# Optimization experiments

Hardware: AMD Instinct MI355X
Metric: run time of the kernel (lower is better)

Reference implementation:

```python
import jax, jax.numpy as jnp
import numpy as np

B, QL, DL = 256, 16, 512      # batch, query len, doc graph nodes
ND, NW, ED = 512, 50000, 300  # n_docs, vocab, embed dim
TOPK, K2, K4 = 40, 240, 192   # args.topk, ggnn2 keep, ggnn4 keep


def setup_inputs() -> dict:
    key = jax.random.key(0)
    ks = jax.random.split(key, 32)
    s = 0.1
    inp = {
        "emb": jax.random.normal(ks[0], (NW + 1, ED), jnp.float32),
        "qrl_token": jax.random.randint(ks[1], (B, QL), 0, NW),
        "doc_token": jax.random.randint(ks[2], (B, DL), 0, NW),
        "doc_ids": jax.random.randint(ks[3], (B,), 0, ND),
        "docs_adj": jax.random.uniform(ks[4], (ND, DL, DL), jnp.float32),
        "idf": jax.random.uniform(ks[5], (B, QL, 1), jnp.float32),
        "W_g1": jax.random.normal(ks[6], (6, QL, QL), jnp.float32) * s,
        "b_g1": jax.random.normal(ks[7], (6, QL), jnp.float32) * s,
        "w_g2": jax.random.normal(ks[8], (6,), jnp.float32) * s,
        "b_g2": jax.random.normal(ks[9], (6,), jnp.float32) * s,
        "W_g3": jax.random.normal(ks[10], (6, QL, QL), jnp.float32) * s,
        "b_g3": jax.random.normal(ks[11], (6, QL), jnp.float32) * s,
        "w_g4": jax.random.normal(ks[12], (6,), jnp.float32) * s,
        "b_g4": jax.random.normal(ks[13], (6,), jnp.float32) * s,
        "p1_w": jax.random.normal(ks[14], (QL,), jnp.float32) * s,
        "p1_b": jax.random.normal(ks[15], (1,), jnp.float32) * s,
        "p2_w": jax.random.normal(ks[16], (QL,), jnp.float32) * s,
        "p2_b": jax.random.normal(ks[17], (1,), jnp.float32) * s,
        "l1_w": jax.random.normal(ks[18], (64, 3 * TOPK), jnp.float32) * s,
        "l1_b": jax.random.normal(ks[19], (64,), jnp.float32) * s,
        "l2_w": jax.random.normal(ks[20], (32, 64), jnp.float32) * s,
        "l2_b": jax.random.normal(ks[21], (32,), jnp.float32) * s,
        "l3_w": jax.random.normal(ks[22], (1, 32), jnp.float32) * s,
        "l3_b": jax.random.normal(ks[23], (1,), jnp.float32) * s,
        "gated_w": jax.random.normal(ks[24], (1,), jnp.float32) * s,
        "gated_b": jax.random.normal(ks[25], (1,), jnp.float32) * s,
    }
    return inp


def _simmat(a_emb, b_emb):
    # cosine similarity [B, A, C]
    an = jnp.linalg.norm(a_emb, axis=2)[:, :, None] + 1e-9
    bn = jnp.linalg.norm(b_emb, axis=2)[:, None, :] + 1e-9
    return jnp.einsum("bad,bcd->bac", a_emb, b_emb) / (an * bn)


def _gate_mat(a, x, W, b):
    # GGNN gated update, W: [6, D, D] stacked (z0,z1,r0,r1,h0,h1)
    lin = lambda t, i: t @ W[i].T + b[i]
    z = jax.nn.sigmoid(lin(a, 0) + lin(x, 1))
    r = jax.nn.sigmoid(lin(a, 2) + lin(x, 3))
    h = jax.nn.relu(lin(a, 4) + lin(r * x, 5))
    return h * z + x * (1.0 - z)


def _gate_scalar(a, x, w, b):
    lin = lambda t, i: t * w[i] + b[i]
    z = jax.nn.sigmoid(lin(a, 0) + lin(x, 1))
    r = jax.nn.sigmoid(lin(a, 2) + lin(x, 3))
    h = jax.nn.relu(lin(a, 4) + lin(r * x, 5))
    return h * z + x * (1.0 - z)


def _sub_adj(A, idx):
    # A: [L, L], idx: [K] -> A[idx][:, idx]
    return A[idx][:, idx]


def reference(emb, qrl_token, doc_token, doc_ids, docs_adj, idf,
              W_g1, b_g1, w_g2, b_g2, W_g3, b_g3, w_g4, b_g4,
              p1_w, p1_b, p2_w, p2_b,
              l1_w, l1_b, l2_w, l2_b, l3_w, l3_b, gated_w, gated_b):
    qe = emb[qrl_token]               # [B, QL, ED]
    de = emb[doc_token]               # [B, DL, ED]
    feat = _simmat(qe, de).transpose(0, 2, 1)   # [B, DL, QL]
    topk0 = jax.lax.top_k(feat.transpose(0, 2, 1), TOPK)[0]  # [B, QL, TOPK]

    adj = docs_adj[doc_ids]           # [B, DL, DL]

    # ggnn1
    rep1 = _gate_mat(adj @ feat, feat, W_g1, b_g1)           # [B, DL, QL]

    # ggnn2 (scalar gates on projected feature + topk subgraph gather)
    x2 = rep1 @ p1_w[:, None] + p1_b                         # [B, DL, 1]
    feat_s = _gate_scalar(adj @ x2, x2, w_g2, b_g2)          # [B, DL, 1]
    score1, idx1 = jax.lax.top_k(feat_s[..., 0], K2)         # [B, K2]
    att_x1 = jnp.take_along_axis(rep1, idx1[:, :, None], axis=1)  # [B, K2, QL]
    adj_new = jax.vmap(_sub_adj)(adj, idx1)                  # [B, K2, K2]
    att_x1 = jnp.tanh(score1)[:, :, None] * att_x1

    # ggnn3
    rep3 = _gate_mat(adj_new @ att_x1, att_x1, W_g3, b_g3)   # [B, K2, QL]

    # ggnn4
    x4 = rep3 @ p2_w[:, None] + p2_b                         # [B, K2, 1]
    feat_s4 = _gate_scalar(adj_new @ x4, x4, w_g4, b_g4)
    score2, idx2 = jax.lax.top_k(feat_s4[..., 0], K4)        # [B, K4]
    att_x2 = jnp.take_along_axis(rep3, idx2[:, :, None], axis=1)  # [B, K4, QL]
    att_x2 = jnp.tanh(score2)[:, :, None] * att_x2

    att1 = jax.lax.top_k(att_x1.transpose(0, 2, 1), TOPK)[0]  # [B, QL, TOPK]
    att2 = jax.lax.top_k(att_x2.transpose(0, 2, 1), TOPK)[0]  # [B, QL, TOPK]
    att_x = jnp.concatenate([topk0, att1, att2], axis=-1)     # [B, QL, 3*TOPK]

    rel = jax.nn.relu(att_x @ l1_w.T + l1_b)
    rel = jax.nn.relu(rel @ l2_w.T + l2_b)
    rel = rel @ l3_w.T + l3_b                                 # [B, QL, 1]

    gated_weight = jax.nn.softmax(idf * gated_w + gated_b, axis=1)
    rel = rel * gated_weight
    scores = rel[..., 0].sum(-1, keepdims=True)               # [B, 1]
    return scores
```

## Files before the change

### kernel.cpp

```cpp
#include <hip/hip_runtime.h>
#include <math.h>

#define B_   256
#define QL_  16
#define DL_  512
#define ED_  300
#define K2_  240
#define K4_  192
#define NEGINF (-3.402823466e38f)

__device__ __forceinline__ float sigf(float x){ return 1.0f/(1.0f+__expf(-x)); }

__device__ __forceinline__ float dot16(const float (&a)[16], const float* w){
  float s = 0.f;
  #pragma unroll
  for (int i=0;i<4;i++){
    float4 ww = *(const float4*)(w + 4*i);
    s = fmaf(a[4*i+0], ww.x, s);
    s = fmaf(a[4*i+1], ww.y, s);
    s = fmaf(a[4*i+2], ww.z, s);
    s = fmaf(a[4*i+3], ww.w, s);
  }
  return s;
}

template<int N, int T>
__device__ void bitonic_desc(float* v, int* id){
  const int tid = threadIdx.x;
  for (int k = 2; k <= N; k <<= 1){
    for (int j = k >> 1; j > 0; j >>= 1){
      __syncthreads();
      for (int i = tid; i < N; i += T){
        const int l = i ^ j;
        if (l > i){
          const float vi = v[i], vl = v[l];
          const int ii = id[i], il = id[l];
          const bool before_l = (vl > vi) || (vl == vi && il < ii);
          const bool up = ((i & k) == 0);
          if (up == before_l){ v[i]=vl; v[l]=vi; id[i]=il; id[l]=ii; }
        }
      }
    }
  }
  __syncthreads();
}

template<int NREG>
__device__ __forceinline__ void wave_sort_desc(float (&v)[NREG], int lane){
  constexpr int TOT = NREG*64;
  #pragma unroll
  for (int k = 2; k <= TOT; k <<= 1){
    #pragma unroll
    for (int j = k>>1; j > 0; j >>= 1){
      if (j >= 64){
        const int jr = j >> 6;
        #pragma unroll
        for (int r = 0; r < NREG; r++){
          if ((r & jr) == 0){
            const int p = r | jr;
            const bool desc = (((r*64) & k) == 0);
            const float a = v[r], c = v[p];
            const float mx = fmaxf(a,c), mn = fminf(a,c);
            v[r] = desc ? mx : mn;
            v[p] = desc ? mn : mx;
          }
        }
      } else {
        #pragma unroll
        for (int r = 0; r < NREG; r++){
          const float ov = __shfl_xor(v[r], j);
          const bool desc = (((r*64 + lane) & k) == 0);
          const bool lower = (lane & j) == 0;
          v[r] = (lower == desc) ? fmaxf(v[r], ov) : fminf(v[r], ov);
        }
      }
    }
  }
}

__global__ __launch_bounds__(1024) void k_all(
    const float* __restrict__ emb, const int* __restrict__ qtok,
    const int* __restrict__ dtok, const int* __restrict__ dids,
    const float* __restrict__ dadj,
    const float* __restrict__ Wg1, const float* __restrict__ bg1,
    const float* __restrict__ p1w, const float* __restrict__ p1b,
    const float* __restrict__ wg2, const float* __restrict__ bg2,
    const float* __restrict__ Wg3, const float* __restrict__ bg3,
    const float* __restrict__ p2w, const float* __restrict__ p2b,
    const float* __restrict__ wg4, const float* __restrict__ bg4,
    const float* __restrict__ l1w, const float* __restrict__ l1b,
    const float* __restrict__ l2w, const float* __restrict__ l2b,
    const float* __restrict__ l3w, const float* __restrict__ l3b,
    const float* __restrict__ idf, const float* __restrict__ gw,
    const float* __restrict__ gb,
    float* __restrict__ adjnew, float* __restrict__ outp)
{
  extern __shared__ float sm[];
  float* ql   = sm;
  float* fx   = ql + 4864;
  float* repl = fx + 10240;
  float* wl   = repl + 10240;
  float* bl   = wl + 1536;
  float* pwl  = bl + 96;
  float* xv   = pwl + 16;
  float* sval = xv + 512;
  int*   sidx = (int*)(sval + 512);
  int*   il   = sidx + 512;
  float* attl = (float*)(il + 240);
  float* rel1 = attl + 1920;
  float* rel2 = rel1 + 1024;
  float* qinv = rel2 + 512;
  int*   toks = (int*)(qinv + 16);

  const int tid = threadIdx.x, b = blockIdx.x;
  const int wave = tid >> 6, lane = tid & 63;
  const float* abase = dadj + (size_t)dids[b]*512*512;

  for (int idx = tid; idx < 16*ED_; idx += 1024){
    const int q = idx / ED_, e = idx - q*ED_;
    ql[q*304+e] = emb[(size_t)qtok[(size_t)b*QL_ + q]*ED_ + e];
  }
  if (tid < 512) toks[tid] = dtok[(size_t)b*DL_ + tid];
  for (int idx = tid; idx < 1536; idx += 1024) wl[idx] = Wg1[idx];
  if (tid >= 1024-96 && tid < 1024) bl[tid-(1024-96)] = bg1[tid-(1024-96)];
  if (tid >= 512 && tid < 528) pwl[tid-512] = p1w[tid-512];
  __syncthreads();
  if (tid < 256){
    const int q = tid >> 4, s = tid & 15;
    float ss = 0.f;
    for (int e=s;e<ED_;e+=16){ const float x = ql[q*304+e]; ss = fmaf(x,x,ss); }
    ss += __shfl_xor(ss,1); ss += __shfl_xor(ss,2);
    ss += __shfl_xor(ss,4); ss += __shfl_xor(ss,8);
    if (s == 0) qinv[q] = 1.f/(sqrtf(ss)+1e-9f);
  }
  __syncthreads();

  {
    const int g = tid>>2, sub = tid&3;
    const float* e0p = emb + (size_t)toks[2*g+0]*ED_;
    const float* e1p = emb + (size_t)toks[2*g+1]*ED_;
    float acc[2][16];
    float ssr[2] = {0.f,0.f};
    #pragma unroll
    for (int r=0;r<2;r++)
      #pragma unroll
      for (int q=0;q<16;q++) acc[r][q] = 0.f;
    for (int i=0;i<19;i++){
      const int j = sub + 4*i;
      if (j < 75){
        const int e0 = 4*j;
        float4 d0v = *(const float4*)(e0p + e0);
        float4 d1v = *(const float4*)(e1p + e0);
        ssr[0] = fmaf(d0v.x,d0v.x, fmaf(d0v.y,d0v.y, fmaf(d0v.z,d0v.z, fmaf(d0v.w,d0v.w, ssr[0]))));
        ssr[1] = fmaf(d1v.x,d1v.x, fmaf(d1v.y,d1v.y, fmaf(d1v.z,d1v.z, fmaf(d1v.w,d1v.w, ssr[1]))));
        #pragma unroll
        for (int q=0;q<16;q++){
          float4 qv = *(const float4*)(&ql[q*304 + e0]);
          acc[0][q] = fmaf(d0v.x,qv.x, fmaf(d0v.y,qv.y, fmaf(d0v.z,qv.z, fmaf(d0v.w,qv.w, acc[0][q]))));
          acc[1][q] = fmaf(d1v.x,qv.x, fmaf(d1v.y,qv.y, fmaf(d1v.z,qv.z, fmaf(d1v.w,qv.w, acc[1][q]))));
        }
      }
    }
    #pragma unroll
    for (int r=0;r<2;r++){
      #pragma unroll
      for (int q=0;q<16;q++){
        float v = acc[r][q];
        v += __shfl_xor(v, 1);
        v += __shfl_xor(v, 2);
        acc[r][q] = v;
      }
      float sv = ssr[r];
      sv += __shfl_xor(sv, 1);
      sv += __shfl_xor(sv, 2);
      ssr[r] = sv;
    }
    if (sub < 2){
      const int d = 2*g + sub;
      const float ssd = sub ? ssr[1] : ssr[0];
      const float invd = 1.f/(sqrtf(ssd)+1e-9f);
      float vs[16];
      #pragma unroll
      for (int q=0;q<16;q++){
        const float v = sub ? acc[1][q] : acc[0][q];
        vs[q] = v * invd * qinv[q];
      }
      float* fo = &fx[(size_t)d*20];
      *(float4*)(fo+0)  = make_float4(vs[0],vs[1],vs[2],vs[3]);
      *(float4*)(fo+4)  = make_float4(vs[4],vs[5],vs[6],vs[7]);
      *(float4*)(fo+8)  = make_float4(vs[8],vs[9],vs[10],vs[11]);
      *(float4*)(fo+12) = make_float4(vs[12],vs[13],vs[14],vs[15]);
    }
  }
  __syncthreads();

  {
    const int q = wave;
    float v[8];
    #pragma unroll
    for (int r=0;r<8;r++) v[r] = fx[(size_t)(lane + 64*r)*20 + q];
    wave_sort_desc<8>(v, lane);
    if (lane < 40) attl[q*120 + lane] = v[0];
  }

  {
    const int g = tid>>2, sub = tid&3;
    const int mb = 2*g;
    const float* r0 = abase + (size_t)mb * 512;
    float acc[2][16];
    #pragma unroll
    for (int r=0;r<2;r++)
      #pragma unroll
      for (int q=0;q<16;q++) acc[r][q] = 0.f;
    for (int i = 0; i < 32; i++){
      const int kk = i*16 + sub*4;
      float4 a0 = *(const float4*)(r0 + kk);
      float4 a1 = *(const float4*)(r0 + 512 + kk);
      const float av[2][4] = {{a0.x,a0.y,a0.z,a0.w},{a1.x,a1.y,a1.z,a1.w}};
      #pragma unroll
      for (int c = 0; c < 4; c++){
        const float* fr = &fx[(size_t)(kk + c)*20];
        float4 q0 = *(const float4*)(fr);
        float4 q1 = *(const float4*)(fr+4);
        float4 q2 = *(const float4*)(fr+8);
        float4 q3 = *(const float4*)(fr+12);
        const float qv[16] = {q0.x,q0.y,q0.z,q0.w, q1.x,q1.y,q1.z,q1.w,
                              q2.x,q2.y,q2.z,q2.w, q3.x,q3.y,q3.z,q3.w};
        #pragma unroll
        for (int r = 0; r < 2; r++){
          const float a_ = av[r][c];
          #pragma unroll
          for (int q = 0; q < 16; q++)
            acc[r][q] = fmaf(a_, qv[q], acc[r][q]);
        }
      }
    }
    #pragma unroll
    for (int r=0;r<2;r++)
      #pragma unroll
      for (int q=0;q<16;q++){
        float v = acc[r][q];
        v += __shfl_xor(v, 1);
        v += __shfl_xor(v, 2);
        acc[r][q] = v;
      }
    if (sub < 2){
      const int m = mb + sub;
      float a[16], x[16];
      #pragma unroll
      for (int q=0;q<16;q++)
        a[q] = sub ? acc[1][q] : acc[0][q];
      {
        const float* xr = &fx[(size_t)m*20];
        float4 x0 = *(const float4*)(xr),   x1 = *(const float4*)(xr+4);
        float4 x2v = *(const float4*)(xr+8), x3 = *(const float4*)(xr+12);
        x[0]=x0.x; x[1]=x0.y; x[2]=x0.z; x[3]=x0.w;
        x[4]=x1.x; x[5]=x1.y; x[6]=x1.z; x[7]=x1.w;
        x[8]=x2v.x; x[9]=x2v.y; x[10]=x2v.z; x[11]=x2v.w;
        x[12]=x3.x; x[13]=x3.y; x[14]=x3.z; x[15]=x3.w;
      }
      float z[16], rr[16];
      #pragma unroll
      for (int q=0;q<16;q++){
        const float s0 = bl[q] + bl[16+q]
                       + dot16(a, &wl[q*16]) + dot16(x, &wl[256 + q*16]);
        z[q] = sigf(s0);
        const float s1 = bl[32+q] + bl[48+q]
                       + dot16(a, &wl[512 + q*16]) + dot16(x, &wl[768 + q*16]);
        rr[q] = sigf(s1);
      }
      float rx[16];
      #pragma unroll
      for (int q=0;q<16;q++) rx[q] = rr[q]*x[q];
      float out[16]; float xp = 0.f;
      #pragma unroll
      for (int q=0;q<16;q++){
        const float s = bl[64+q] + bl[80+q]
                      + dot16(a, &wl[1024 + q*16]) + dot16(rx, &wl[1280 + q*16]);
        const float h = fmaxf(s, 0.f);
        const float o = h*z[q] + x[q]*(1.f - z[q]);
        out[q] = o;
        xp = fmaf(o, pwl[q], xp);
      }
      float* rp = &repl[(size_t)m*20];
      *(float4*)(rp+0)  = make_float4(out[0],out[1],out[2],out[3]);
      *(float4*)(rp+4)  = make_float4(out[4],out[5],out[6],out[7]);
      *(float4*)(rp+8)  = make_float4(out[8],out[9],out[10],out[11]);
      *(float4*)(rp+12) = make_float4(out[12],out[13],out[14],out[15]);
      xv[m] = xp + p1b[0];
    }
  }
  __syncthreads();

  {
    const int g = tid >> 2, sub = tid & 3;
    const float w0=wg2[0],w1=wg2[1],w2=wg2[2],w3=wg2[3],w4=wg2[4],w5=wg2[5];
    const float c0=bg2[0],c1=bg2[1],c2=bg2[2],c3=bg2[3],c4=bg2[4],c5=bg2[5];
    #pragma unroll
    for (int pp=0; pp<2; pp++){
      const int m = pp*256 + g;
      const float* row = abase + (size_t)m*512;
      float s = 0.f;
      #pragma unroll
      for (int ii=0; ii<8; ii++){
        const int k0 = ii*64 + sub*4;
        float4 a0 = *(const float4*)(row + k0);
        float4 a1 = *(const float4*)(row + k0 + 16);
        float4 a2 = *(const float4*)(row + k0 + 32);
        float4 a3 = *(const float4*)(row + k0 + 48);
        float4 x0 = *(const float4*)(&xv[k0]);
        float4 x1 = *(const float4*)(&xv[k0+16]);
        float4 x2v = *(const float4*)(&xv[k0+32]);
        float4 x3 = *(const float4*)(&xv[k0+48]);
        s = fmaf(a0.x,x0.x,s); s = fmaf(a0.y,x0.y,s);
        s = fmaf(a0.z,x0.z,s); s = fmaf(a0.w,x0.w,s);
        s = fmaf(a1.x,x1.x,s); s = fmaf(a1.y,x1.y,s);
        s = fmaf(a1.z,x1.z,s); s = fmaf(a1.w,x1.w,s);
        s = fmaf(a2.x,x2v.x,s); s = fmaf(a2.y,x2v.y,s);
        s = fmaf(a2.z,x2v.z,s); s = fmaf(a2.w,x2v.w,s);
        s = fmaf(a3.x,x3.x,s); s = fmaf(a3.y,x3.y,s);
        s = fmaf(a3.z,x3.z,s); s = fmaf(a3.w,x3.w,s);
      }
      s += __shfl_xor(s,1); s += __shfl_xor(s,2);
      if (sub == 0){
        const float x = xv[m];
        const float z = sigf(fmaf(s,w0,c0) + fmaf(x,w1,c1));
        const float r = sigf(fmaf(s,w2,c2) + fmaf(x,w3,c3));
        const float h = fmaxf(fmaf(s,w4,c4) + fmaf(r*x,w5,c5), 0.f);
        sval[m] = h*z + x*(1.f - z);
        sidx[m] = m;
      }
    }
  }
  bitonic_desc<512,1024>(sval, sidx);

  if (tid < K2_){
    const int rowi = sidx[tid];
    il[tid] = rowi;
    const float tv = tanhf(sval[tid]);
    const float* rr = &repl[(size_t)rowi*20];
    float4 r0 = *(const float4*)(rr),   r1 = *(const float4*)(rr+4);
    float4 r2 = *(const float4*)(rr+8), r3 = *(const float4*)(rr+12);
    float* o = &fx[(size_t)tid*20];
    *(float4*)(o+0)  = make_float4(tv*r0.x,tv*r0.y,tv*r0.z,tv*r0.w);
    *(float4*)(o+4)  = make_float4(tv*r1.x,tv*r1.y,tv*r1.z,tv*r1.w);
    *(float4*)(o+8)  = make_float4(tv*r2.x,tv*r2.y,tv*r2.z,tv*r2.w);
    *(float4*)(o+12) = make_float4(tv*r3.x,tv*r3.y,tv*r3.z,tv*r3.w);
  }
  __syncthreads();

  if (wave < 12){
    int jc[4];
    #pragma unroll
    for (int c=0;c<4;c++){
      const int j = lane + 64*c;
      jc[c] = (j < K2_) ? il[j] : 0;
    }
    #pragma unroll
    for (int p=0;p<20;p++){
      const int r = wave*20 + p;
      const float* row = abase + (size_t)il[r]*512;
      float* orow = adjnew + ((size_t)b*K2_ + r)*K2_;
      #pragma unroll
      for (int c=0;c<4;c++){
        const int j = lane + 64*c;
        if (j < K2_) orow[j] = row[jc[c]];
      }
    }
  } else {
    const int t4 = tid - 768;
    for (int idx = t4; idx < 1536; idx += 256) wl[idx] = Wg3[idx];
    if (t4 < 96) bl[t4] = bg3[t4];
    if (t4 < 16) pwl[t4] = p2w[t4];
    #pragma unroll
    for (int t=0;t<4;t++){
      const int q = (wave-12)*4 + t;
      float v[4];
      #pragma unroll
      for (int r=0;r<4;r++){
        const int idx = lane + 64*r;
        v[r] = (idx < K2_) ? fx[(size_t)idx*20 + q] : NEGINF;
      }
      wave_sort_desc<4>(v, lane);
      if (lane < 40) attl[q*120 + 40 + lane] = v[0];
    }
  }
  __syncthreads();

  {
    const int g = tid >> 2, sub = tid & 3;
    if (g < K2_){
      const int m = g;
      const float* r0 = adjnew + ((size_t)b*K2_ + m)*K2_;
      float acc[16];
      #pragma unroll
      for (int q=0;q<16;q++) acc[q] = 0.f;
      for (int i=0;i<15;i++){
        const int kk = i*16 + sub*4;
        float4 a4 = *(const float4*)(r0 + kk);
        const float av[4] = {a4.x, a4.y, a4.z, a4.w};
        #pragma unroll
        for (int c=0;c<4;c++){
          const float* fr = &fx[(size_t)(kk + c)*20];
          float4 q0 = *(const float4*)(fr);
          float4 q1 = *(const float4*)(fr+4);
          float4 q2 = *(const float4*)(fr+8);
          float4 q3 = *(const float4*)(fr+12);
          const float qv[16] = {q0.x,q0.y,q0.z,q0.w, q1.x,q1.y,q1.z,q1.w,
                                q2.x,q2.y,q2.z,q2.w, q3.x,q3.y,q3.z,q3.w};
          #pragma unroll
          for (int q=0;q<16;q++)
            acc[q] = fmaf(av[c], qv[q], acc[q]);
        }
      }
      #pragma unroll
      for (int q=0;q<16;q++){
        float v = acc[q];
        v += __shfl_xor(v, 1);
        v += __shfl_xor(v, 2);
        acc[q] = v;
      }
      float x[16];
      {
        const float* xr = &fx[(size_t)m*20];
        float4 x0 = *(const float4*)(xr),   x1 = *(const float4*)(xr+4);
        float4 x2v = *(const float4*)(xr+8), x3 = *(const float4*)(xr+12);
        x[0]=x0.x; x[1]=x0.y; x[2]=x0.z; x[3]=x0.w;
        x[4]=x1.x; x[5]=x1.y; x[6]=x1.z; x[7]=x1.w;
        x[8]=x2v.x; x[9]=x2v.y; x[10]=x2v.z; x[11]=x2v.w;
        x[12]=x3.x; x[13]=x3.y; x[14]=x3.z; x[15]=x3.w;
      }
      float rx[16];
      #pragma unroll
      for (int q=0;q<16;q++){
        const float s1 = bl[32+q] + bl[48+q]
                       + dot16(acc, &wl[512 + q*16]) + dot16(x, &wl[768 + q*16]);
        rx[q] = sigf(s1) * x[q];
      }
      float xp = 0.f;
      #pragma unroll
      for (int j=0;j<4;j++){
        const int q = sub*4 + j;
        const float s0 = bl[q] + bl[16+q]
                       + dot16(acc, &wl[q*16]) + dot16(x, &wl[256 + q*16]);
        const float z = sigf(s0);
        const float s = bl[64+q] + bl[80+q]
                      + dot16(acc, &wl[1024 + q*16]) + dot16(rx, &wl[1280 + q*16]);
        const float h = fmaxf(s, 0.f);
        const float o = h*z + x[q]*(1.f - z);
        repl[(size_t)m*20 + q] = o;
        xp = fmaf(o, pwl[q], xp);
      }
      xp += __shfl_xor(xp,1); xp += __shfl_xor(xp,2);
      if (sub == 0) xv[m] = xp + p2b[0];
    }
  }
  __syncthreads();

  {
    const int g = tid >> 2, sub = tid & 3;
    const float w0=wg4[0],w1=wg4[1],w2=wg4[2],w3=wg4[3],w4=wg4[4],w5=wg4[5];
    const float c0=bg4[0],c1=bg4[1],c2=bg4[2],c3=bg4[3],c4=bg4[4],c5=bg4[5];
    if (g < K2_){
      const float* row = adjnew + ((size_t)b*K2_ + g)*K2_;
      float s = 0.f;
      #pragma unroll
      for (int i=0;i<15;i++){
        const int kk = i*16 + sub*4;
        float4 a4 = *(const float4*)(row + kk);
        float4 xq = *(const float4*)(&xv[kk]);
        s = fmaf(a4.x,xq.x,s); s = fmaf(a4.y,xq.y,s);
        s = fmaf(a4.z,xq.z,s); s = fmaf(a4.w,xq.w,s);
      }
      s += __shfl_xor(s,1); s += __shfl_xor(s,2);
      if (sub == 0){
        const float x = xv[g];
        const float z = sigf(fmaf(s,w0,c0) + fmaf(x,w1,c1));
        const float r = sigf(fmaf(s,w2,c2) + fmaf(x,w3,c3));
        const float h = fmaxf(fmaf(s,w4,c4) + fmaf(r*x,w5,c5), 0.f);
        sval[g] = h*z + x*(1.f - z);
        sidx[g] = g;
      }
    }
    if (tid >= 960 && tid < 976){
      sval[K2_ + tid - 960] = NEGINF;
      sidx[K2_ + tid - 960] = 0x7fffffff;
    }
  }
  bitonic_desc<256,1024>(sval, sidx);

  if (tid < K4_){
    const int rowi = sidx[tid];
    const float tv = tanhf(sval[tid]);
    const float* rr = &repl[(size_t)rowi*20];
    float4 r0 = *(const float4*)(rr),   r1 = *(const float4*)(rr+4);
    float4 r2 = *(const float4*)(rr+8), r3 = *(const float4*)(rr+12);
    float* o = &fx[(size_t)tid*20];
    *(float4*)(o+0)  = make_float4(tv*r0.x,tv*r0.y,tv*r0.z,tv*r0.w);
    *(float4*)(o+4)  = make_float4(tv*r1.x,tv*r1.y,tv*r1.z,tv*r1.w);
    *(float4*)(o+8)  = make_float4(tv*r2.x,tv*r2.y,tv*r2.z,tv*r2.w);
    *(float4*)(o+12) = make_float4(tv*r3.x,tv*r3.y,tv*r3.z,tv*r3.w);
  }
  __syncthreads();

  {
    const int q = wave;
    float v[4];
    #pragma unroll
    for (int r=0;r<4;r++){
      const int idx = lane + 64*r;
      v[r] = (idx < K4_) ? fx[(size_t)idx*20 + q] : NEGINF;
    }
    wave_sort_desc<4>(v, lane);
    if (lane < 40) attl[q*120 + 80 + lane] = v[0];
  }
  __syncthreads();

  {
    const int q = tid >> 6, u = tid & 63;
    float acc = l1b[u];
    const float* wrow = l1w + (size_t)u*120;
    #pragma unroll
    for (int k4=0;k4<30;k4++){
      float4 av = *(const float4*)(&attl[q*120 + k4*4]);
      float4 wv = *(const float4*)(wrow + k4*4);
      acc = fmaf(av.x,wv.x,acc); acc = fmaf(av.y,wv.y,acc);
      acc = fmaf(av.z,wv.z,acc); acc = fmaf(av.w,wv.w,acc);
    }
    rel1[q*64 + u] = fmaxf(acc, 0.f);
  }
  __syncthreads();
  if (tid < 512){
    const int q = tid >> 5, u = tid & 31;
    float acc = l2b[u];
    const float* wrow = l2w + (size_t)u*64;
    #pragma unroll
    for (int k4=0;k4<16;k4++){
      float4 av = *(const float4*)(&rel1[q*64 + k4*4]);
      float4 wv = *(const float4*)(wrow + k4*4);
      acc = fmaf(av.x,wv.x,acc); acc = fmaf(av.y,wv.y,acc);
      acc = fmaf(av.z,wv.z,acc); acc = fmaf(av.w,wv.w,acc);
    }
    rel2[q*32 + u] = fmaxf(acc, 0.f);
  }
  __syncthreads();
  if (tid < 16){
    float acc = l3b[0];
    #pragma unroll
    for (int k=0;k<32;k++) acc = fmaf(rel2[tid*32+k], l3w[k], acc);
    const float gv = fmaf(idf[(size_t)b*16 + tid], gw[0], gb[0]);
    float mx = gv;
    mx = fmaxf(mx, __shfl_xor(mx, 1));
    mx = fmaxf(mx, __shfl_xor(mx, 2));
    mx = fmaxf(mx, __shfl_xor(mx, 4));
    mx = fmaxf(mx, __shfl_xor(mx, 8));
    const float e = __expf(gv - mx);
    float se = e;
    se += __shfl_xor(se, 1); se += __shfl_xor(se, 2);
    se += __shfl_xor(se, 4); se += __shfl_xor(se, 8);
    float val = acc * (e / se);
    val += __shfl_xor(val, 1); val += __shfl_xor(val, 2);
    val += __shfl_xor(val, 4); val += __shfl_xor(val, 8);
    if (tid == 0) outp[b] = val;
  }
}

extern "C" void kernel_launch(void* const* d_in, const int* in_sizes, int n_in,
                              void* d_out, int out_size, void* d_ws, size_t ws_size,
                              hipStream_t stream)
{
  const float* emb  = (const float*)d_in[0];
  const int*   qtok = (const int*)d_in[1];
  const int*   dtok = (const int*)d_in[2];
  const int*   dids = (const int*)d_in[3];
  const float* dadj = (const float*)d_in[4];
  const float* idf  = (const float*)d_in[5];
  const float* Wg1  = (const float*)d_in[6];
  const float* bg1  = (const float*)d_in[7];
  const float* wg2  = (const float*)d_in[8];
  const float* bg2  = (const float*)d_in[9];
  const float* Wg3  = (const float*)d_in[10];
  const float* bg3  = (const float*)d_in[11];
  const float* wg4  = (const float*)d_in[12];
  const float* bg4  = (const float*)d_in[13];
  const float* p1w  = (const float*)d_in[14];
  const float* p1b  = (const float*)d_in[15];
  const float* p2w  = (const float*)d_in[16];
  const float* p2b  = (const float*)d_in[17];
  const float* l1w  = (const float*)d_in[18];
  const float* l1b  = (const float*)d_in[19];
  const float* l2w  = (const float*)d_in[20];
  const float* l2b  = (const float*)d_in[21];
  const float* l3w  = (const float*)d_in[22];
  const float* l3b  = (const float*)d_in[23];
  const float* gw   = (const float*)d_in[24];
  const float* gb   = (const float*)d_in[25];
  float* out = (float*)d_out;

  float* adjnew = (float*)d_ws;

  const size_t lds_bytes = 32740u * 4u;

  k_all<<<B_, 1024, lds_bytes, stream>>>(
      emb, qtok, dtok, dids, dadj,
      Wg1, bg1, p1w, p1b, wg2, bg2, Wg3, bg3, p2w, p2b, wg4, bg4,
      l1w, l1b, l2w, l2b, l3w, l3b, idf, gw, gb,
      adjnew, out);
}
```

Baseline: 235.3 us.

## Prefetch embedding and adjacency rows, specialize waves for GGNN1 versus top-k sort

Embedding row loads in the similarity stage are software-pipelined two iterations ahead. The GGNN1 adjacency matmul is now done by the first 8 waves, each thread group handling 4 rows with a one-step register prefetch. The remaining waves run the per-query top-k sorts (two queries each) at the same time, so the work is split across waves instead of running in sequence. This raises register pressure (4x16 accumulators) and cuts the number of waves doing the matmul, which risks lower occupancy and longer GGNN1 time. The prefetch in the embedding loop also reads past the valid range on the last iterations, which may touch memory beyond the row.

Result: slower. 283.3 us (+20.4%).

```diff
diff --git a/kernel.cpp b/kernel.cpp
--- a/kernel.cpp
+++ b/kernel.cpp
@@ -145,21 +145,27 @@
     for (int r=0;r<2;r++)
       #pragma unroll
       for (int q=0;q<16;q++) acc[r][q] = 0.f;
+    float4 a0 = *(const float4*)(e0p + 4*(sub));
+    float4 a1 = *(const float4*)(e1p + 4*(sub));
+    float4 b0 = *(const float4*)(e0p + 4*(sub+4));
+    float4 b1 = *(const float4*)(e1p + 4*(sub+4));
     for (int i=0;i<19;i++){
+      const int jn = sub + 4*(i+2);
+      float4 c0v = *(const float4*)(e0p + 4*jn);
+      float4 c1v = *(const float4*)(e1p + 4*jn);
       const int j = sub + 4*i;
       if (j < 75){
         const int e0 = 4*j;
-        float4 d0v = *(const float4*)(e0p + e0);
-        float4 d1v = *(const float4*)(e1p + e0);
-        ssr[0] = fmaf(d0v.x,d0v.x, fmaf(d0v.y,d0v.y, fmaf(d0v.z,d0v.z, fmaf(d0v.w,d0v.w, ssr[0]))));
-        ssr[1] = fmaf(d1v.x,d1v.x, fmaf(d1v.y,d1v.y, fmaf(d1v.z,d1v.z, fmaf(d1v.w,d1v.w, ssr[1]))));
+        ssr[0] = fmaf(a0.x,a0.x, fmaf(a0.y,a0.y, fmaf(a0.z,a0.z, fmaf(a0.w,a0.w, ssr[0]))));
+        ssr[1] = fmaf(a1.x,a1.x, fmaf(a1.y,a1.y, fmaf(a1.z,a1.z, fmaf(a1.w,a1.w, ssr[1]))));
         #pragma unroll
         for (int q=0;q<16;q++){
           float4 qv = *(const float4*)(&ql[q*304 + e0]);
-          acc[0][q] = fmaf(d0v.x,qv.x, fmaf(d0v.y,qv.y, fmaf(d0v.z,qv.z, fmaf(d0v.w,qv.w, acc[0][q]))));
-          acc[1][q] = fmaf(d1v.x,qv.x, fmaf(d1v.y,qv.y, fmaf(d1v.z,qv.z, fmaf(d1v.w,qv.w, acc[1][q]))));
+          acc[0][q] = fmaf(a0.x,qv.x, fmaf(a0.y,qv.y, fmaf(a0.z,qv.z, fmaf(a0.w,qv.w, acc[0][q]))));
+          acc[1][q] = fmaf(a1.x,qv.x, fmaf(a1.y,qv.y, fmaf(a1.z,qv.z, fmaf(a1.w,qv.w, acc[1][q]))));
         }
       }
+      a0 = b0; a1 = b1; b0 = c0v; b1 = c1v;
     }
     #pragma unroll
     for (int r=0;r<2;r++){
@@ -194,29 +200,28 @@
   }
   __syncthreads();
 
-  {
-    const int q = wave;
-    float v[8];
-    #pragma unroll
-    for (int r=0;r<8;r++) v[r] = fx[(size_t)(lane + 64*r)*20 + q];
-    wave_sort_desc<8>(v, lane);
-    if (lane < 40) attl[q*120 + lane] = v[0];
-  }
-
-  {
-    const int g = tid>>2, sub = tid&3;
-    const int mb = 2*g;
+  if (wave < 8){
+    const int g = tid >> 2, sub = tid & 3;
+    const int mb = 4*g;
     const float* r0 = abase + (size_t)mb * 512;
-    float acc[2][16];
-    #pragma unroll
-    for (int r=0;r<2;r++)
+    float acc[4][16];
+    #pragma unroll
+    for (int r=0;r<4;r++)
       #pragma unroll
       for (int q=0;q<16;q++) acc[r][q] = 0.f;
+    int kk = sub*4;
+    float4 c0 = *(const float4*)(r0 + kk);
+    float4 c1 = *(const float4*)(r0 + 512 + kk);
+    float4 c2 = *(const float4*)(r0 + 2*512 + kk);
+    float4 c3 = *(const float4*)(r0 + 3*512 + kk);
     for (int i = 0; i < 32; i++){
-      const int kk = i*16 + sub*4;
-      float4 a0 = *(const float4*)(r0 + kk);
-      float4 a1 = *(const float4*)(r0 + 512 + kk);
-      const float av[2][4] = {{a0.x,a0.y,a0.z,a0.w},{a1.x,a1.y,a1.z,a1.w}};
+      const int kn = kk + ((i < 31) ? 16 : 0);
+      float4 n0 = *(const float4*)(r0 + kn);
+      float4 n1 = *(const float4*)(r0 + 512 + kn);
+      float4 n2 = *(const float4*)(r0 + 2*512 + kn);
+      float4 n3 = *(const float4*)(r0 + 3*512 + kn);
+      const float av[4][4] = {{c0.x,c0.y,c0.z,c0.w},{c1.x,c1.y,c1.z,c1.w},
+                              {c2.x,c2.y,c2.z,c2.w},{c3.x,c3.y,c3.z,c3.w}};
       #pragma unroll
       for (int c = 0; c < 4; c++){
         const float* fr = &fx[(size_t)(kk + c)*20];
@@ -227,16 +232,18 @@
         const float qv[16] = {q0.x,q0.y,q0.z,q0.w, q1.x,q1.y,q1.z,q1.w,
                               q2.x,q2.y,q2.z,q2.w, q3.x,q3.y,q3.z,q3.w};
         #pragma unroll
-        for (int r = 0; r < 2; r++){
+        for (int r = 0; r < 4; r++){
           const float a_ = av[r][c];
           #pragma unroll
           for (int q = 0; q < 16; q++)
             acc[r][q] = fmaf(a_, qv[q], acc[r][q]);
         }
       }
-    }
-    #pragma unroll
-    for (int r=0;r<2;r++)
+      c0 = n0; c1 = n1; c2 = n2; c3 = n3;
+      kk += 16;
+    }
+    #pragma unroll
+    for (int r=0;r<4;r++)
       #pragma unroll
       for (int q=0;q<16;q++){
         float v = acc[r][q];
@@ -244,50 +251,58 @@
         v += __shfl_xor(v, 2);
         acc[r][q] = v;
       }
-    if (sub < 2){
-      const int m = mb + sub;
-      float a[16], x[16];
-      #pragma unroll
-      for (int q=0;q<16;q++)
-        a[q] = sub ? acc[1][q] : acc[0][q];
-      {
-        const float* xr = &fx[(size_t)m*20];
-        float4 x0 = *(const float4*)(xr),   x1 = *(const float4*)(xr+4);
-        float4 x2v = *(const float4*)(xr+8), x3 = *(const float4*)(xr+12);
-        x[0]=x0.x; x[1]=x0.y; x[2]=x0.z; x[3]=x0.w;
-        x[4]=x1.x; x[5]=x1.y; x[6]=x1.z; x[7]=x1.w;
-        x[8]=x2v.x; x[9]=x2v.y; x[10]=x2v.z; x[11]=x2v.w;
-        x[12]=x3.x; x[13]=x3.y; x[14]=x3.z; x[15]=x3.w;
-      }
-      float z[16], rr[16];
-      #pragma unroll
-      for (int q=0;q<16;q++){
-        const float s0 = bl[q] + bl[16+q]
-                       + dot16(a, &wl[q*16]) + dot16(x, &wl[256 + q*16]);
-        z[q] = sigf(s0);
-        const float s1 = bl[32+q] + bl[48+q]
-                       + dot16(a, &wl[512 + q*16]) + dot16(x, &wl[768 + q*16]);
-        rr[q] = sigf(s1);
-      }
-      float rx[16];
-      #pragma unroll
-      for (int q=0;q<16;q++) rx[q] = rr[q]*x[q];
-      float out[16]; float xp = 0.f;
-      #pragma unroll
-      for (int q=0;q<16;q++){
-        const float s = bl[64+q] + bl[80+q]
-                      + dot16(a, &wl[1024 + q*16]) + dot16(rx, &wl[1280 + q*16]);
-        const float h = fmaxf(s, 0.f);
-        const float o = h*z[q] + x[q]*(1.f - z[q]);
-        out[q] = o;
-        xp = fmaf(o, pwl[q], xp);
-      }
-      float* rp = &repl[(size_t)m*20];
-      *(float4*)(rp+0)  = make_float4(out[0],out[1],out[2],out[3]);
-      *(float4*)(rp+4)  = make_float4(out[4],out[5],out[6],out[7]);
-      *(float4*)(rp+8)  = make_float4(out[8],out[9],out[10],out[11]);
-      *(float4*)(rp+12) = make_float4(out[12],out[13],out[14],out[15]);
-      xv[m] = xp + p1b[0];
+    const int m = mb + sub;
+    float a[16], x[16];
+    #pragma unroll
+    for (int q=0;q<16;q++)
+      a[q] = (sub==0)?acc[0][q]:(sub==1)?acc[1][q]:(sub==2)?acc[2][q]:acc[3][q];
+    {
+      const float* xr = &fx[(size_t)m*20];
+      float4 x0 = *(const float4*)(xr),   x1 = *(const float4*)(xr+4);
+      float4 x2v = *(const float4*)(xr+8), x3 = *(const float4*)(xr+12);
+      x[0]=x0.x; x[1]=x0.y; x[2]=x0.z; x[3]=x0.w;
+      x[4]=x1.x; x[5]=x1.y; x[6]=x1.z; x[7]=x1.w;
+      x[8]=x2v.x; x[9]=x2v.y; x[10]=x2v.z; x[11]=x2v.w;
+      x[12]=x3.x; x[13]=x3.y; x[14]=x3.z; x[15]=x3.w;
+    }
+    float z[16], rr[16];
+    #pragma unroll
+    for (int q=0;q<16;q++){
+      const float s0 = bl[q] + bl[16+q]
+                     + dot16(a, &wl[q*16]) + dot16(x, &wl[256 + q*16]);
+      z[q] = sigf(s0);
+      const float s1 = bl[32+q] + bl[48+q]
+                     + dot16(a, &wl[512 + q*16]) + dot16(x, &wl[768 + q*16]);
+      rr[q] = sigf(s1);
+    }
+    float rx[16];
+    #pragma unroll
+    for (int q=0;q<16;q++) rx[q] = rr[q]*x[q];
+    float out[16]; float xp = 0.f;
+    #pragma unroll
+    for (int q=0;q<16;q++){
+      const float s = bl[64+q] + bl[80+q]
+                    + dot16(a, &wl[1024 + q*16]) + dot16(rx, &wl[1280 + q*16]);
+      const float h = fmaxf(s, 0.f);
+      const float o = h*z[q] + x[q]*(1.f - z[q]);
+      out[q] = o;
+      xp = fmaf(o, pwl[q], xp);
+    }
+    float* rp = &repl[(size_t)m*20];
+    *(float4*)(rp+0)  = make_float4(out[0],out[1],out[2],out[3]);
+    *(float4*)(rp+4)  = make_float4(out[4],out[5],out[6],out[7]);
+    *(float4*)(rp+8)  = make_float4(out[8],out[9],out[10],out[11]);
+    *(float4*)(rp+12) = make_float4(out[12],out[13],out[14],out[15]);
+    xv[m] = xp + p1b[0];
+  } else {
+    #pragma unroll
+    for (int t=0;t<2;t++){
+      const int q = (wave-8)*2 + t;
+      float v[8];
+      #pragma unroll
+      for (int r=0;r<8;r++) v[r] = fx[(size_t)(lane + 64*r)*20 + q];
+      wave_sort_desc<8>(v, lane);
+      if (lane < 40) attl[q*120 + lane] = v[0];
     }
   }
   __syncthreads();
```

## Use register/shuffle hybrid bitonic sort and transposed LDS buffers for top-k

Applied to the files above, without the earlier changes.

The shared-memory bitonic sort, which synchronised on every stage, is replaced by a register-held sort. Partner exchanges with stride below 64 use wave shuffles and only larger strides go through LDS with barriers. The per-column top-k reads also switch from a stride-20 row layout to transposed padded buffers (stride 513/241) to avoid LDS bank conflicts. This costs extra LDS (the allocation grows) and extra scatter stores when the transposes are written.

Measured after the change: 234.3 us. Within noise of the previous version (-0.4%).

```diff
diff --git a/kernel.cpp b/kernel.cpp
--- a/kernel.cpp
+++ b/kernel.cpp
@@ -24,24 +24,40 @@
   return s;
 }
 
-template<int N, int T>
-__device__ void bitonic_desc(float* v, int* id){
+template<int N>
+__device__ void hybrid_sort(float* sval, int* sidx){
   const int tid = threadIdx.x;
+  const bool act = (tid < N);
+  __syncthreads();
+  float v = NEGINF; int id = 0x7fffffff;
+  if (act){ v = sval[tid]; id = sidx[tid]; }
   for (int k = 2; k <= N; k <<= 1){
     for (int j = k >> 1; j > 0; j >>= 1){
-      __syncthreads();
-      for (int i = tid; i < N; i += T){
-        const int l = i ^ j;
-        if (l > i){
-          const float vi = v[i], vl = v[l];
-          const int ii = id[i], il = id[l];
-          const bool before_l = (vl > vi) || (vl == vi && il < ii);
-          const bool up = ((i & k) == 0);
-          if (up == before_l){ v[i]=vl; v[l]=vi; id[i]=il; id[l]=ii; }
+      if (j >= 64){
+        if (act){ sval[tid] = v; sidx[tid] = id; }
+        __syncthreads();
+        if (act){
+          const int p = tid ^ j;
+          const float ov = sval[p]; const int oid = sidx[p];
+          const bool obm = (ov > v) || (ov == v && oid < id);
+          const bool lower = (tid & j) == 0;
+          const bool desc = (tid & k) == 0;
+          if (obm ^ (lower != desc)){ v = ov; id = oid; }
         }
-      }
-    }
-  }
+        __syncthreads();
+      } else {
+        if (act){
+          const float ov = __shfl_xor(v, j);
+          const int oid = __shfl_xor(id, j);
+          const bool obm = (ov > v) || (ov == v && oid < id);
+          const bool lower = (tid & j) == 0;
+          const bool desc = (tid & k) == 0;
+          if (obm ^ (lower != desc)){ v = ov; id = oid; }
+        }
+      }
+    }
+  }
+  if (act){ sval[tid] = v; sidx[tid] = id; }
   __syncthreads();
 }
 
@@ -96,25 +112,27 @@
     float* __restrict__ adjnew, float* __restrict__ outp)
 {
   extern __shared__ float sm[];
-  float* ql   = sm;
-  float* fx   = ql + 4864;
-  float* repl = fx + 10240;
-  float* wl   = repl + 10240;
-  float* bl   = wl + 1536;
-  float* pwl  = bl + 96;
-  float* xv   = pwl + 16;
-  float* sval = xv + 512;
-  int*   sidx = (int*)(sval + 512);
-  int*   il   = sidx + 512;
-  float* attl = (float*)(il + 240);
-  float* rel1 = attl + 1920;
-  float* rel2 = rel1 + 1024;
-  float* qinv = rel2 + 512;
-  int*   toks = (int*)(qinv + 16);
+  float* ql     = sm;
+  float* fx     = ql + 4864;
+  float* repl   = fx + 10240;
+  float* wl     = repl + 10240;
+  float* bl     = wl + 1536;
+  float* pwl    = bl + 96;
+  float* xv     = pwl + 16;
+  float* sval   = xv + 512;
+  int*   sidx   = (int*)(sval + 512);
+  int*   il     = sidx + 512;
+  float* attl   = (float*)(il + 240);
+  float* rel1   = attl + 1920;
+  float* rel2   = rel1 + 1024;
+  float* qinv   = rel2 + 512;
+  int*   toks   = (int*)(qinv + 16);
+  float* attx1T = (float*)(toks + 512);
 
   const int tid = threadIdx.x, b = blockIdx.x;
   const int wave = tid >> 6, lane = tid & 63;
   const float* abase = dadj + (size_t)dids[b]*512*512;
+  float* fxT = repl;
 
   for (int idx = tid; idx < 16*ED_; idx += 1024){
     const int q = idx / ED_, e = idx - q*ED_;
@@ -190,6 +208,8 @@
       *(float4*)(fo+4)  = make_float4(vs[4],vs[5],vs[6],vs[7]);
       *(float4*)(fo+8)  = make_float4(vs[8],vs[9],vs[10],vs[11]);
       *(float4*)(fo+12) = make_float4(vs[12],vs[13],vs[14],vs[15]);
+      #pragma unroll
+      for (int q=0;q<16;q++) fxT[q*513 + d] = vs[q];
     }
   }
   __syncthreads();
@@ -198,10 +218,11 @@
     const int q = wave;
     float v[8];
     #pragma unroll
-    for (int r=0;r<8;r++) v[r] = fx[(size_t)(lane + 64*r)*20 + q];
+    for (int r=0;r<8;r++) v[r] = fxT[q*513 + lane + 64*r];
     wave_sort_desc<8>(v, lane);
     if (lane < 40) attl[q*120 + lane] = v[0];
   }
+  __syncthreads();
 
   {
     const int g = tid>>2, sub = tid&3;
@@ -332,7 +353,7 @@
       }
     }
   }
-  bitonic_desc<512,1024>(sval, sidx);
+  hybrid_sort<512>(sval, sidx);
 
   if (tid < K2_){
     const int rowi = sidx[tid];
@@ -341,11 +362,17 @@
     const float* rr = &repl[(size_t)rowi*20];
     float4 r0 = *(const float4*)(rr),   r1 = *(const float4*)(rr+4);
     float4 r2 = *(const float4*)(rr+8), r3 = *(const float4*)(rr+12);
+    const float vv[16] = {tv*r0.x,tv*r0.y,tv*r0.z,tv*r0.w,
+                          tv*r1.x,tv*r1.y,tv*r1.z,tv*r1.w,
+                          tv*r2.x,tv*r2.y,tv*r2.z,tv*r2.w,
+                          tv*r3.x,tv*r3.y,tv*r3.z,tv*r3.w};
     float* o = &fx[(size_t)tid*20];
-    *(float4*)(o+0)  = make_float4(tv*r0.x,tv*r0.y,tv*r0.z,tv*r0.w);
-    *(float4*)(o+4)  = make_float4(tv*r1.x,tv*r1.y,tv*r1.z,tv*r1.w);
-    *(float4*)(o+8)  = make_float4(tv*r2.x,tv*r2.y,tv*r2.z,tv*r2.w);
-    *(float4*)(o+12) = make_float4(tv*r3.x,tv*r3.y,tv*r3.z,tv*r3.w);
+    *(float4*)(o+0)  = make_float4(vv[0],vv[1],vv[2],vv[3]);
+    *(float4*)(o+4)  = make_float4(vv[4],vv[5],vv[6],vv[7]);
+    *(float4*)(o+8)  = make_float4(vv[8],vv[9],vv[10],vv[11]);
+    *(float4*)(o+12) = make_float4(vv[12],vv[13],vv[14],vv[15]);
+    #pragma unroll
+    for (int q=0;q<16;q++) attx1T[q*241 + tid] = vv[q];
   }
   __syncthreads();
 
@@ -379,7 +406,7 @@
       #pragma unroll
       for (int r=0;r<4;r++){
         const int idx = lane + 64*r;
-        v[r] = (idx < K2_) ? fx[(size_t)idx*20 + q] : NEGINF;
+        v[r] = (idx < K2_) ? attx1T[q*241 + idx] : NEGINF;
       }
       wave_sort_desc<4>(v, lane);
       if (lane < 40) attl[q*120 + 40 + lane] = v[0];
@@ -487,7 +514,7 @@
       sidx[K2_ + tid - 960] = 0x7fffffff;
     }
   }
-  bitonic_desc<256,1024>(sval, sidx);
+  hybrid_sort<256>(sval, sidx);
 
   if (tid < K4_){
     const int rowi = sidx[tid];
@@ -495,11 +522,12 @@
     const float* rr = &repl[(size_t)rowi*20];
     float4 r0 = *(const float4*)(rr),   r1 = *(const float4*)(rr+4);
     float4 r2 = *(const float4*)(rr+8), r3 = *(const float4*)(rr+12);
-    float* o = &fx[(size_t)tid*20];
-    *(float4*)(o+0)  = make_float4(tv*r0.x,tv*r0.y,tv*r0.z,tv*r0.w);
-    *(float4*)(o+4)  = make_float4(tv*r1.x,tv*r1.y,tv*r1.z,tv*r1.w);
-    *(float4*)(o+8)  = make_float4(tv*r2.x,tv*r2.y,tv*r2.z,tv*r2.w);
-    *(float4*)(o+12) = make_float4(tv*r3.x,tv*r3.y,tv*r3.z,tv*r3.w);
+    const float vv[16] = {tv*r0.x,tv*r0.y,tv*r0.z,tv*r0.w,
+                          tv*r1.x,tv*r1.y,tv*r1.z,tv*r1.w,
+                          tv*r2.x,tv*r2.y,tv*r2.z,tv*r2.w,
+                          tv*r3.x,tv*r3.y,tv*r3.z,tv*r3.w};
+    #pragma unroll
+    for (int q=0;q<16;q++) attx1T[q*241 + tid] = vv[q];
   }
   __syncthreads();
 
@@ -509,7 +537,7 @@
     #pragma unroll
     for (int r=0;r<4;r++){
       const int idx = lane + 64*r;
-      v[r] = (idx < K4_) ? fx[(size_t)idx*20 + q] : NEGINF;
+      v[r] = (idx < K4_) ? attx1T[q*241 + idx] : NEGINF;
     }
     wave_sort_desc<4>(v, lane);
     if (lane < 40) attl[q*120 + 80 + lane] = v[0];
@@ -599,7 +627,7 @@
 
   float* adjnew = (float*)d_ws;
 
-  const size_t lds_bytes = 32740u * 4u;
+  const size_t lds_bytes = 36608u * 4u;
 
   k_all<<<B_, 1024, lds_bytes, stream>>>(
       emb, qtok, dtok, dids, dadj,
```
